# Optimization experiments

Measured on AMD Instinct MI355X. Metric: run time of the kernel, lower is better.

The kernel has to match this reference:

```python
import jax, jax.numpy as jnp
import numpy as np

# res_scale = (max(scale)+float_scale)/max(scale) = 2.5/2 = 1.25
RES_SCALE = 1.25


def _dct(x):
    # DCT-II via FFT (Makhoul), norm=None, matching torch module's dct().
    # x: [..., N]
    N = x.shape[-1]
    v = jnp.concatenate([x[..., ::2], x[..., 1::2][..., ::-1]], axis=-1)
    Vc = jnp.fft.fft(v, axis=-1)  # full FFT == _rfft(onesided=False)
    k = -jnp.arange(N, dtype=x.dtype) * (np.pi / (2.0 * N))
    V = 2.0 * (Vc.real * jnp.cos(k) - Vc.imag * jnp.sin(k))
    return V.astype(x.dtype)


def _idct(X):
    # Inverse of DCT-II (norm=None), matching torch module's idct().
    # X: [..., N]
    N = X.shape[-1]
    Xv = X / 2.0
    k = jnp.arange(N, dtype=X.dtype) * (np.pi / (2.0 * N))
    Wr, Wi = jnp.cos(k), jnp.sin(k)
    Vt_r = Xv
    Vt_i = jnp.concatenate([jnp.zeros_like(Xv[..., :1]), -Xv[..., ::-1][..., :-1]], axis=-1)
    V_r = Vt_r * Wr - Vt_i * Wi
    V_i = Vt_r * Wi + Vt_i * Wr
    # _irfft(onesided=False): keep first N//2+1 bins, irfft back to length N
    Vc = (V_r[..., : N // 2 + 1] + 1j * V_i[..., : N // 2 + 1]).astype(jnp.complex64)
    v = jnp.fft.irfft(Vc, n=N, axis=-1).astype(X.dtype)
    # odd/even de-shuffle
    x = jnp.zeros_like(v)
    x = x.at[..., ::2].set(v[..., : N - N // 2])
    x = x.at[..., 1::2].set(v[..., ::-1][..., : N // 2])
    return x


def _dct_2d(x):
    return jnp.swapaxes(_dct(jnp.swapaxes(_dct(x), -1, -2)), -1, -2)


def _idct_2d(X):
    return jnp.swapaxes(_idct(jnp.swapaxes(_idct(X), -1, -2)), -1, -2)


def setup_inputs() -> dict:
    key = jax.random.key(0)
    x = jax.random.normal(key, (16, 3, 768, 768), dtype=jnp.float32)
    return {"x": x}


def reference(x):
    B, C, H, W = x.shape
    outH, outW = int(H * RES_SCALE), int(W * RES_SCALE)
    X = _dct_2d(x)
    # ZeroPad2d((0, outW-W, 0, outH-H)): pad right and bottom with zeros
    X = jnp.pad(X, ((0, 0), (0, 0), (0, outH - H), (0, outW - W)))
    return _idct_2d(X)
```

## Files before the change

### kernel.cpp

```cpp
#include <hip/hip_runtime.h>


#define HW 768
#define OHW 960
#define NIMG 48

typedef __attribute__((ext_vector_type(8))) short short8;
typedef __attribute__((ext_vector_type(4))) float f32x4;
typedef __attribute__((ext_vector_type(4))) float float4v;
typedef __attribute__((ext_vector_type(4))) unsigned short us4;

__device__ __forceinline__ unsigned short f2bf(float f) {
    union { float f; unsigned int u; } v; v.f = f;
    unsigned int u = v.u;
    return (unsigned short)((u + 0x7FFFu + ((u >> 16) & 1u)) >> 16);
}

__device__ __forceinline__ void glds16(const void* g, void* l) {
    __builtin_amdgcn_global_load_lds(
        (const __attribute__((address_space(1))) void*)g,
        (__attribute__((address_space(3))) void*)l, 16, 0, 0);
}

__device__ __forceinline__ float dsum(int p) {
    int n1 = (767 * p) % 30720;
    int n2 = (768 * p) % 30720;
    const float w = (float)(3.14159265358979323846 / 15360.0);
    return sinf((float)n1 * w) * cosf((float)n2 * w) / sinf((float)p * w);
}

__global__ void fill_M(unsigned short* __restrict__ Mb) {
    int idx = blockIdx.x * 256 + threadIdx.x;
    if (idx >= OHW * HW) return;
    int i = idx / HW, n = idx - i * HW;
    int a = 8 * i + 4, b = 10 * n + 5;
    int p1 = a + b;
    int p2 = a - b; if (p2 < 0) p2 += 15360;
    float m = (1.0f + dsum(p1) + dsum(p2)) * (1.0f / 960.0f);
    Mb[idx] = f2bf(m);
}

__global__ void conv_bf16(const float* __restrict__ x, unsigned short* __restrict__ xb, int n4) {
    int i = blockIdx.x * 256 + threadIdx.x;
    if (i >= n4) return;
    float4v v = *(const float4v*)(x + (size_t)i * 4);
    us4 o; o.x = f2bf(v.x); o.y = f2bf(v.y); o.z = f2bf(v.z); o.w = f2bf(v.w);
    *(us4*)(xb + (size_t)i * 4) = o;
}

__global__ __launch_bounds__(256) void gemm_bt(
    const unsigned short* __restrict__ A, int lda,
    const unsigned short* __restrict__ Bg, long long strideB, int ldb,
    void* __restrict__ Cg, long long strideC, int ldc,
    int Md, int Nd, int Kd, int out_f32)
{
    __shared__ unsigned short As[128 * 32];
    __shared__ unsigned short Bs[128 * 32];

    const int tid = threadIdx.x;
    const int wave = tid >> 6, lane = tid & 63;
    const int wm = wave >> 1, wn = wave & 1;
    const int t16 = lane & 15, quad = lane >> 4;
    const int z = blockIdx.z;

    const unsigned short* B = Bg + (size_t)z * strideB;
    const int mb = blockIdx.y * 128, nbb = blockIdx.x * 128;

    f32x4 acc[4][4];
#pragma unroll
    for (int i = 0; i < 4; ++i)
#pragma unroll
        for (int j = 0; j < 4; ++j)
            acc[i][j] = (f32x4){0.f, 0.f, 0.f, 0.f};

    const int rowT = tid >> 2;
    const int ksw = (((tid & 3) ^ ((rowT >> 1) & 3)) << 3);
    unsigned short* lA0 = As + wave * 512;
    unsigned short* lB0 = Bs + wave * 512;

    int grA0 = mb + rowT;        if (grA0 >= Md) grA0 = Md - 1;
    int grA1 = mb + rowT + 64;   if (grA1 >= Md) grA1 = Md - 1;
    int gnB0 = nbb + rowT;       if (gnB0 >= Nd) gnB0 = Nd - 1;
    int gnB1 = nbb + rowT + 64;  if (gnB1 >= Nd) gnB1 = Nd - 1;
    const unsigned short* pA0 = A + (size_t)grA0 * lda + ksw;
    const unsigned short* pA1 = A + (size_t)grA1 * lda + ksw;
    const unsigned short* pB0 = B + (size_t)gnB0 * ldb + ksw;
    const unsigned short* pB1 = B + (size_t)gnB1 * ldb + ksw;

    const int quadx = quad ^ ((t16 >> 1) & 3);
    const int aBase = (wm * 64 + t16) * 32 + quadx * 8;
    const int bBase = (wn * 64 + t16) * 32 + quadx * 8;

    for (int k0 = 0; k0 < Kd; k0 += 32) {
        glds16(pA0 + k0, lA0);
        glds16(pA1 + k0, lA0 + 2048);
        glds16(pB0 + k0, lB0);
        glds16(pB1 + k0, lB0 + 2048);
        __syncthreads();

        short8 af[4], bfr[4];
#pragma unroll
        for (int mi = 0; mi < 4; ++mi)
            af[mi] = *(const short8*)(&As[aBase + mi * 512]);
#pragma unroll
        for (int ni = 0; ni < 4; ++ni)
            bfr[ni] = *(const short8*)(&Bs[bBase + ni * 512]);
#pragma unroll
        for (int mi = 0; mi < 4; ++mi)
#pragma unroll
            for (int ni = 0; ni < 4; ++ni)
                acc[mi][ni] = __builtin_amdgcn_mfma_f32_16x16x32_bf16(
                    af[mi], bfr[ni], acc[mi][ni], 0, 0, 0);
        __syncthreads();
    }

    const int gr0 = mb + wm * 64;
    const int gc0 = nbb + wn * 64;
    if (out_f32) {
        float* C = (float*)Cg + (size_t)z * strideC;
#pragma unroll
        for (int mi = 0; mi < 4; ++mi)
#pragma unroll
            for (int ni = 0; ni < 4; ++ni) {
                int col = gc0 + ni * 16 + t16;
                if (col < Nd) {
#pragma unroll
                    for (int r = 0; r < 4; ++r) {
                        int rowg = gr0 + mi * 16 + quad * 4 + r;
                        if (rowg < Md) C[(size_t)rowg * ldc + col] = acc[mi][ni][r];
                    }
                }
            }
    } else {
        unsigned short* C = (unsigned short*)Cg + (size_t)z * strideC;
#pragma unroll
        for (int mi = 0; mi < 4; ++mi)
#pragma unroll
            for (int ni = 0; ni < 4; ++ni) {
                int col = gc0 + ni * 16 + t16;
                if (col < Nd) {
#pragma unroll
                    for (int r = 0; r < 4; ++r) {
                        int rowg = gr0 + mi * 16 + quad * 4 + r;
                        if (rowg < Md) C[(size_t)rowg * ldc + col] = f2bf(acc[mi][ni][r]);
                    }
                }
            }
    }
}

extern "C" void kernel_launch(void* const* d_in, const int* in_sizes, int n_in,
                              void* d_out, int out_size, void* d_ws, size_t ws_size,
                              hipStream_t stream) {
    const float* x = (const float*)d_in[0];
    float* out = (float*)d_out;
    char* ws = (char*)d_ws;

    size_t offM  = 0;
    size_t fixed = offM + (size_t)OHW * HW * 2;
    size_t perImg = (size_t)HW * HW * 2 + (size_t)OHW * HW * 2;

    int nb = 1;
    if (ws_size > fixed + perImg) {
        size_t q = (ws_size - fixed) / perImg;
        nb = (q > 48) ? 48 : (int)q;
        if (nb < 1) nb = 1;
    }

    unsigned short* Mb = (unsigned short*)(ws + offM);
    unsigned short* xb = (unsigned short*)(ws + fixed);
    unsigned short* T  = (unsigned short*)(ws + fixed + (size_t)nb * HW * HW * 2);

    fill_M<<<(OHW * HW + 255) / 256, 256, 0, stream>>>(Mb);

    for (int b0 = 0; b0 < NIMG; b0 += nb) {
        int cur = NIMG - b0; if (cur > nb) cur = nb;
        int n4 = cur * (HW * HW / 4);
        conv_bf16<<<(n4 + 255) / 256, 256, 0, stream>>>(
            x + (size_t)b0 * HW * HW, xb, n4);
        gemm_bt<<<dim3(6, 8, cur), 256, 0, stream>>>(
            Mb, HW, xb, (long long)HW * HW, HW,
            T, (long long)OHW * HW, HW, OHW, HW, HW, 0);
        gemm_bt<<<dim3(8, 8, cur), 256, 0, stream>>>(
            Mb, HW, T, (long long)OHW * HW, HW,
            out + (size_t)b0 * OHW * OHW, (long long)OHW * OHW, OHW,
            OHW, OHW, HW, 1);
    }
    (void)in_sizes; (void)n_in; (void)out_size;
}
```

Before: 425.7 us.

## Double-buffer LDS tiles with K=64 steps in bf16 GEMM

The GEMM main loop now uses two LDS buffers with 64-wide K tiles and issues global-to-LDS loads for the next tile while MFMAs run on the current one. This halves the number of barriers per K and overlaps memory latency with compute. LDS use grows to 64 KB per block, which can lower occupancy. The loop assumes the K tile count is even, which holds for K=768.

```diff
diff --git a/kernel.cpp b/kernel.cpp
--- a/kernel.cpp
+++ b/kernel.cpp
@@ -54,8 +54,8 @@
     void* __restrict__ Cg, long long strideC, int ldc,
     int Md, int Nd, int Kd, int out_f32)
 {
-    __shared__ unsigned short As[128 * 32];
-    __shared__ unsigned short Bs[128 * 32];
+    __shared__ unsigned short As[2][128 * 64];
+    __shared__ unsigned short Bs[2][128 * 64];
 
     const int tid = threadIdx.x;
     const int wave = tid >> 6, lane = tid & 63;
@@ -63,7 +63,7 @@
     const int t16 = lane & 15, quad = lane >> 4;
     const int z = blockIdx.z;
 
-    const unsigned short* B = Bg + (size_t)z * strideB;
+    const unsigned short* Bp = Bg + (size_t)z * strideB;
     const int mb = blockIdx.y * 128, nbb = blockIdx.x * 128;
 
     f32x4 acc[4][4];
@@ -73,46 +73,74 @@
         for (int j = 0; j < 4; ++j)
             acc[i][j] = (f32x4){0.f, 0.f, 0.f, 0.f};
 
-    const int rowT = tid >> 2;
-    const int ksw = (((tid & 3) ^ ((rowT >> 1) & 3)) << 3);
-    unsigned short* lA0 = As + wave * 512;
-    unsigned short* lB0 = Bs + wave * 512;
-
-    int grA0 = mb + rowT;        if (grA0 >= Md) grA0 = Md - 1;
-    int grA1 = mb + rowT + 64;   if (grA1 >= Md) grA1 = Md - 1;
-    int gnB0 = nbb + rowT;       if (gnB0 >= Nd) gnB0 = Nd - 1;
-    int gnB1 = nbb + rowT + 64;  if (gnB1 >= Nd) gnB1 = Nd - 1;
-    const unsigned short* pA0 = A + (size_t)grA0 * lda + ksw;
-    const unsigned short* pA1 = A + (size_t)grA1 * lda + ksw;
-    const unsigned short* pB0 = B + (size_t)gnB0 * ldb + ksw;
-    const unsigned short* pB1 = B + (size_t)gnB1 * ldb + ksw;
-
-    const int quadx = quad ^ ((t16 >> 1) & 3);
-    const int aBase = (wm * 64 + t16) * 32 + quadx * 8;
-    const int bBase = (wn * 64 + t16) * 32 + quadx * 8;
-
-    for (int k0 = 0; k0 < Kd; k0 += 32) {
-        glds16(pA0 + k0, lA0);
-        glds16(pA1 + k0, lA0 + 2048);
-        glds16(pB0 + k0, lB0);
-        glds16(pB1 + k0, lB0 + 2048);
+    const int srow = tid >> 3;
+    const int klog = (((tid & 7) ^ ((tid >> 4) & 7))) * 8;
+    const unsigned short* pA[4];
+    const unsigned short* pB[4];
+#pragma unroll
+    for (int j = 0; j < 4; ++j) {
+        int ra = mb + srow + 32 * j;  if (ra >= Md) ra = Md - 1;
+        int rb = nbb + srow + 32 * j; if (rb >= Nd) rb = Nd - 1;
+        pA[j] = A  + (size_t)ra * lda + klog;
+        pB[j] = Bp + (size_t)rb * ldb + klog;
+    }
+    unsigned short* dA = &As[0][0] + tid * 8;
+    unsigned short* dB = &Bs[0][0] + tid * 8;
+
+    const int swz = (t16 >> 1) & 7;
+    int aOff[2], bOff[2];
+#pragma unroll
+    for (int ks = 0; ks < 2; ++ks) {
+        int ph = ((ks * 4 + quad) ^ swz) * 8;
+        aOff[ks] = (wm * 64 + t16) * 64 + ph;
+        bOff[ks] = (wn * 64 + t16) * 64 + ph;
+    }
+
+#define STAGE(buf, kt) do {                                                   \
+    int kk_ = (kt) * 64;                                                      \
+    _Pragma("unroll")                                                         \
+    for (int j_ = 0; j_ < 4; ++j_)                                            \
+        glds16(pA[j_] + kk_, dA + (buf) * 8192 + j_ * 2048);                  \
+    _Pragma("unroll")                                                         \
+    for (int j_ = 0; j_ < 4; ++j_)                                            \
+        glds16(pB[j_] + kk_, dB + (buf) * 8192 + j_ * 2048);                  \
+} while (0)
+
+#define COMPUTE(buf) do {                                                     \
+    _Pragma("unroll")                                                         \
+    for (int ks_ = 0; ks_ < 2; ++ks_) {                                       \
+        short8 af_[4], bf_[4];                                                \
+        _Pragma("unroll")                                                     \
+        for (int mi_ = 0; mi_ < 4; ++mi_)                                     \
+            af_[mi_] = *(const short8*)(&As[buf][0] + aOff[ks_] + mi_ * 1024);\
+        _Pragma("unroll")                                                     \
+        for (int ni_ = 0; ni_ < 4; ++ni_)                                     \
+            bf_[ni_] = *(const short8*)(&Bs[buf][0] + bOff[ks_] + ni_ * 1024);\
+        _Pragma("unroll")                                                     \
+        for (int mi_ = 0; mi_ < 4; ++mi_)                                     \
+        _Pragma("unroll")                                                     \
+        for (int ni_ = 0; ni_ < 4; ++ni_)                                     \
+            acc[mi_][ni_] = __builtin_amdgcn_mfma_f32_16x16x32_bf16(          \
+                af_[mi_], bf_[ni_], acc[mi_][ni_], 0, 0, 0);                  \
+    }                                                                         \
+} while (0)
+
+    const int NT = Kd >> 6;
+
+    STAGE(0, 0);
+    __syncthreads();
+
+    for (int kt = 0; kt + 2 <= NT; kt += 2) {
+        STAGE(1, kt + 1);
+        COMPUTE(0);
         __syncthreads();
-
-        short8 af[4], bfr[4];
-#pragma unroll
-        for (int mi = 0; mi < 4; ++mi)
-            af[mi] = *(const short8*)(&As[aBase + mi * 512]);
-#pragma unroll
-        for (int ni = 0; ni < 4; ++ni)
-            bfr[ni] = *(const short8*)(&Bs[bBase + ni * 512]);
-#pragma unroll
-        for (int mi = 0; mi < 4; ++mi)
-#pragma unroll
-            for (int ni = 0; ni < 4; ++ni)
-                acc[mi][ni] = __builtin_amdgcn_mfma_f32_16x16x32_bf16(
-                    af[mi], bfr[ni], acc[mi][ni], 0, 0, 0);
+        if (kt + 2 < NT) STAGE(0, kt + 2);
+        COMPUTE(1);
         __syncthreads();
     }
+
+#undef STAGE
+#undef COMPUTE
 
     const int gr0 = mb + wm * 64;
     const int gc0 = nbb + wn * 64;
```

Result: no change. 419.9 us (-1.4%).

## Rewrite GEMM as persistent 256x256-tile kernel with double-buffered LDS pipeline

Applied to the files above, without the earlier changes.

Replaces the 128x128 single-buffered GEMM with a persistent-grid kernel using 256x256 tiles, 512 threads, and BK=64 double-buffered LDS. Global-to-LDS loads for the next k-step, or the next tile at the end of the loop, overlap MFMA work through interleaved fragment reads, raw barriers and setprio hints. The goal is more data reuse per load and less barrier stall. In exchange it uses much more LDS and more accumulator registers. The M buffer is padded by 64 rows because the 256-row tiles read past row 960.

```diff
diff --git a/kernel.cpp b/kernel.cpp
--- a/kernel.cpp
+++ b/kernel.cpp
@@ -4,6 +4,7 @@
 #define HW 768
 #define OHW 960
 #define NIMG 48
+#define NTILES 12
 
 typedef __attribute__((ext_vector_type(8))) short short8;
 typedef __attribute__((ext_vector_type(4))) float f32x4;
@@ -48,104 +49,169 @@
     *(us4*)(xb + (size_t)i * 4) = o;
 }
 
-__global__ __launch_bounds__(256) void gemm_bt(
+#define ASM_BAR   asm volatile("s_barrier" ::: "memory")
+#define ASM_VM0   asm volatile("s_waitcnt vmcnt(0)" ::: "memory")
+
+__global__ __launch_bounds__(512, 2) void gemm_bt(
     const unsigned short* __restrict__ A, int lda,
     const unsigned short* __restrict__ Bg, long long strideB, int ldb,
     void* __restrict__ Cg, long long strideC, int ldc,
-    int Md, int Nd, int Kd, int out_f32)
+    int Md, int Nd, int out_f32, int gx, int gy, int nA)
 {
-    __shared__ unsigned short As[128 * 32];
-    __shared__ unsigned short Bs[128 * 32];
+    __shared__ unsigned short As[2][256 * 64];
+    __shared__ unsigned short Bs[2][256 * 64];
 
     const int tid = threadIdx.x;
     const int wave = tid >> 6, lane = tid & 63;
-    const int wm = wave >> 1, wn = wave & 1;
+    const int wm = wave >> 2, wn = wave & 3;
     const int t16 = lane & 15, quad = lane >> 4;
-    const int z = blockIdx.z;
-
-    const unsigned short* B = Bg + (size_t)z * strideB;
-    const int mb = blockIdx.y * 128, nbb = blockIdx.x * 128;
-
-    f32x4 acc[4][4];
-#pragma unroll
-    for (int i = 0; i < 4; ++i)
+    const int nB = gridDim.x;
+
+    int a = blockIdx.x;
+    if (a >= nA) return;
+
+    const int srow = tid >> 3;
+    const int klog = ((tid & 7) ^ ((tid >> 4) & 7)) * 8;
+    int invA[4], invB[4];
+#pragma unroll
+    for (int j = 0; j < 4; ++j) {
+        invA[j] = (srow + 64 * j) * lda + klog;
+        invB[j] = (srow + 64 * j) * ldb + klog;
+    }
+    const int dOff = tid * 8;
+
+    const int swz = (t16 >> 1) & 7;
+    const int ph0 = (quad ^ swz) * 8;
+    const int ph1 = ((4 + quad) ^ swz) * 8;
+    const int aRow = (wm * 128 + t16) * 64;
+    const int bRow = (wn * 64 + t16) * 64;
+
+    f32x4 acc[8][4];
+#pragma unroll
+    for (int i = 0; i < 8; ++i)
 #pragma unroll
         for (int j = 0; j < 4; ++j)
             acc[i][j] = (f32x4){0.f, 0.f, 0.f, 0.f};
 
-    const int rowT = tid >> 2;
-    const int ksw = (((tid & 3) ^ ((rowT >> 1) & 3)) << 3);
-    unsigned short* lA0 = As + wave * 512;
-    unsigned short* lB0 = Bs + wave * 512;
-
-    int grA0 = mb + rowT;        if (grA0 >= Md) grA0 = Md - 1;
-    int grA1 = mb + rowT + 64;   if (grA1 >= Md) grA1 = Md - 1;
-    int gnB0 = nbb + rowT;       if (gnB0 >= Nd) gnB0 = Nd - 1;
-    int gnB1 = nbb + rowT + 64;  if (gnB1 >= Nd) gnB1 = Nd - 1;
-    const unsigned short* pA0 = A + (size_t)grA0 * lda + ksw;
-    const unsigned short* pA1 = A + (size_t)grA1 * lda + ksw;
-    const unsigned short* pB0 = B + (size_t)gnB0 * ldb + ksw;
-    const unsigned short* pB1 = B + (size_t)gnB1 * ldb + ksw;
-
-    const int quadx = quad ^ ((t16 >> 1) & 3);
-    const int aBase = (wm * 64 + t16) * 32 + quadx * 8;
-    const int bBase = (wn * 64 + t16) * 32 + quadx * 8;
-
-    for (int k0 = 0; k0 < Kd; k0 += 32) {
-        glds16(pA0 + k0, lA0);
-        glds16(pA1 + k0, lA0 + 2048);
-        glds16(pB0 + k0, lB0);
-        glds16(pB1 + k0, lB0 + 2048);
-        __syncthreads();
-
-        short8 af[4], bfr[4];
-#pragma unroll
-        for (int mi = 0; mi < 4; ++mi)
-            af[mi] = *(const short8*)(&As[aBase + mi * 512]);
-#pragma unroll
-        for (int ni = 0; ni < 4; ++ni)
-            bfr[ni] = *(const short8*)(&Bs[bBase + ni * 512]);
-#pragma unroll
-        for (int mi = 0; mi < 4; ++mi)
-#pragma unroll
-            for (int ni = 0; ni < 4; ++ni)
-                acc[mi][ni] = __builtin_amdgcn_mfma_f32_16x16x32_bf16(
-                    af[mi], bfr[ni], acc[mi][ni], 0, 0, 0);
-        __syncthreads();
-    }
-
-    const int gr0 = mb + wm * 64;
-    const int gc0 = nbb + wn * 64;
-    if (out_f32) {
-        float* C = (float*)Cg + (size_t)z * strideC;
-#pragma unroll
-        for (int mi = 0; mi < 4; ++mi)
-#pragma unroll
-            for (int ni = 0; ni < 4; ++ni) {
-                int col = gc0 + ni * 16 + t16;
-                if (col < Nd) {
-#pragma unroll
-                    for (int r = 0; r < 4; ++r) {
-                        int rowg = gr0 + mi * 16 + quad * 4 + r;
-                        if (rowg < Md) C[(size_t)rowg * ldc + col] = acc[mi][ni][r];
+    int mb, nbb, zz; long long offA, offB;
+#define DECODE(aa) do { int gxy_ = gx * gy; zz = (aa) / gxy_;                  \
+    int r_ = (aa) - zz * gxy_; int by_ = r_ / gx; int bx_ = r_ - by_ * gx;     \
+    mb = by_ * 256; nbb = bx_ * 256;                                           \
+    offA = (long long)mb * lda;                                                \
+    offB = (long long)zz * strideB + (long long)nbb * ldb; } while (0)
+
+    DECODE(a);
+
+#define STG_A(buf, stk) do { _Pragma("unroll")                                 \
+    for (int j_ = 0; j_ < 4; ++j_)                                             \
+        glds16(A + offA + invA[j_] + (stk),                                    \
+               &As[buf][0] + dOff + j_ * 4096); } while (0)
+#define STG_B(buf, stk) do { _Pragma("unroll")                                 \
+    for (int j_ = 0; j_ < 4; ++j_)                                             \
+        glds16(Bg + offB + invB[j_] + (stk),                                   \
+               &Bs[buf][0] + dOff + j_ * 4096); } while (0)
+
+    short8 afr0[4][2], afr1[4][2], bf0[2][2], bf1[2][2];
+
+#define RD_A(dst, base, mig) do { _Pragma("unroll")                            \
+    for (int mi_ = 0; mi_ < 4; ++mi_) {                                        \
+        dst[mi_][0] = *(const short8*)((base) + aRow + ((mig)*4+mi_)*1024 + ph0); \
+        dst[mi_][1] = *(const short8*)((base) + aRow + ((mig)*4+mi_)*1024 + ph1); \
+    } } while (0)
+#define RD_B(dst, base, nig) do { _Pragma("unroll")                            \
+    for (int ni_ = 0; ni_ < 2; ++ni_) {                                        \
+        dst[ni_][0] = *(const short8*)((base) + bRow + ((nig)*2+ni_)*1024 + ph0); \
+        dst[ni_][1] = *(const short8*)((base) + bRow + ((nig)*2+ni_)*1024 + ph1); \
+    } } while (0)
+
+#define MMA_Q(mig, nig, av, bv) do {                                           \
+    __builtin_amdgcn_s_setprio(1);                                             \
+    _Pragma("unroll")                                                          \
+    for (int ks_ = 0; ks_ < 2; ++ks_)                                          \
+    _Pragma("unroll")                                                          \
+    for (int mi_ = 0; mi_ < 4; ++mi_)                                          \
+    _Pragma("unroll")                                                          \
+    for (int ni_ = 0; ni_ < 2; ++ni_)                                          \
+        acc[(mig)*4+mi_][(nig)*2+ni_] =                                        \
+            __builtin_amdgcn_mfma_f32_16x16x32_bf16(                           \
+                av[mi_][ks_], bv[ni_][ks_],                                    \
+                acc[(mig)*4+mi_][(nig)*2+ni_], 0, 0, 0);                       \
+    __builtin_amdgcn_s_setprio(0); } while (0)
+
+    STG_A(0, 0); STG_B(0, 0);
+    ASM_VM0; ASM_BAR;
+    RD_A(afr0, &As[0][0], 0);
+    RD_B(bf0, &Bs[0][0], 0);
+
+    for (;;) {
+        const int emb = mb, enb = nbb, ez = zz;
+#pragma unroll 2
+        for (int t = 0; t < NTILES; ++t) {
+            const int c = t & 1, n = c ^ 1;
+            const unsigned short* Asc = &As[c][0];
+            const unsigned short* Bsc = &Bs[c][0];
+            bool pf = true; int stk = (t + 1) * 64;
+            if (t == NTILES - 1) {
+                if (a + nB < nA) { DECODE(a + nB); stk = 0; }
+                else pf = false;
+            }
+            if (pf) STG_A(n, stk);
+            RD_B(bf1, Bsc, 1);
+            MMA_Q(0, 0, afr0, bf0);
+            ASM_BAR;
+            if (pf) STG_B(n, stk);
+            RD_A(afr1, Asc, 1);
+            MMA_Q(0, 1, afr0, bf1);
+            ASM_BAR;
+            MMA_Q(1, 0, afr1, bf0);
+            ASM_VM0;
+            ASM_BAR;
+            if (pf) { RD_A(afr0, &As[n][0], 0); RD_B(bf0, &Bs[n][0], 0); }
+            MMA_Q(1, 1, afr1, bf1);
+            ASM_BAR;
+        }
+
+        const int gr0 = emb + wm * 128;
+        const int gc0 = enb + wn * 64;
+        if (out_f32) {
+            float* C = (float*)Cg + (size_t)ez * strideC;
+#pragma unroll
+            for (int mi = 0; mi < 8; ++mi)
+#pragma unroll
+                for (int ni = 0; ni < 4; ++ni) {
+                    int col = gc0 + ni * 16 + t16;
+                    if (col < Nd) {
+#pragma unroll
+                        for (int r = 0; r < 4; ++r) {
+                            int rowg = gr0 + mi * 16 + quad * 4 + r;
+                            if (rowg < Md) C[(size_t)rowg * ldc + col] = acc[mi][ni][r];
+                        }
                     }
                 }
-            }
-    } else {
-        unsigned short* C = (unsigned short*)Cg + (size_t)z * strideC;
-#pragma unroll
-        for (int mi = 0; mi < 4; ++mi)
-#pragma unroll
-            for (int ni = 0; ni < 4; ++ni) {
-                int col = gc0 + ni * 16 + t16;
-                if (col < Nd) {
-#pragma unroll
-                    for (int r = 0; r < 4; ++r) {
-                        int rowg = gr0 + mi * 16 + quad * 4 + r;
-                        if (rowg < Md) C[(size_t)rowg * ldc + col] = f2bf(acc[mi][ni][r]);
+        } else {
+            unsigned short* C = (unsigned short*)Cg + (size_t)ez * strideC;
+#pragma unroll
+            for (int mi = 0; mi < 8; ++mi)
+#pragma unroll
+                for (int ni = 0; ni < 4; ++ni) {
+                    int col = gc0 + ni * 16 + t16;
+                    if (col < Nd) {
+#pragma unroll
+                        for (int r = 0; r < 4; ++r) {
+                            int rowg = gr0 + mi * 16 + quad * 4 + r;
+                            if (rowg < Md) C[(size_t)rowg * ldc + col] = f2bf(acc[mi][ni][r]);
+                        }
                     }
                 }
-            }
+        }
+
+        a += nB;
+        if (a >= nA) break;
+#pragma unroll
+        for (int i = 0; i < 8; ++i)
+#pragma unroll
+            for (int j = 0; j < 4; ++j)
+                acc[i][j] = (f32x4){0.f, 0.f, 0.f, 0.f};
     }
 }
 
@@ -156,20 +222,22 @@
     float* out = (float*)d_out;
     char* ws = (char*)d_ws;
 
-    size_t offM  = 0;
-    size_t fixed = offM + (size_t)OHW * HW * 2;
-    size_t perImg = (size_t)HW * HW * 2 + (size_t)OHW * HW * 2;
+    size_t szM   = (size_t)(OHW + 64) * HW * 2;
+    size_t fixed = szM;
+    size_t perImgX = (size_t)HW * HW * 2;
+    size_t perImgT = (size_t)OHW * HW * 2;
+    size_t padT  = (size_t)64 * HW * 2;
 
     int nb = 1;
-    if (ws_size > fixed + perImg) {
-        size_t q = (ws_size - fixed) / perImg;
+    if (ws_size > fixed + perImgX + perImgT + padT) {
+        size_t q = (ws_size - fixed - padT) / (perImgX + perImgT);
         nb = (q > 48) ? 48 : (int)q;
         if (nb < 1) nb = 1;
     }
 
-    unsigned short* Mb = (unsigned short*)(ws + offM);
+    unsigned short* Mb = (unsigned short*)(ws + 0);
     unsigned short* xb = (unsigned short*)(ws + fixed);
-    unsigned short* T  = (unsigned short*)(ws + fixed + (size_t)nb * HW * HW * 2);
+    unsigned short* T  = (unsigned short*)(ws + fixed + (size_t)nb * perImgX);
 
     fill_M<<<(OHW * HW + 255) / 256, 256, 0, stream>>>(Mb);
 
@@ -178,13 +246,21 @@
         int n4 = cur * (HW * HW / 4);
         conv_bf16<<<(n4 + 255) / 256, 256, 0, stream>>>(
             x + (size_t)b0 * HW * HW, xb, n4);
-        gemm_bt<<<dim3(6, 8, cur), 256, 0, stream>>>(
-            Mb, HW, xb, (long long)HW * HW, HW,
-            T, (long long)OHW * HW, HW, OHW, HW, HW, 0);
-        gemm_bt<<<dim3(8, 8, cur), 256, 0, stream>>>(
-            Mb, HW, T, (long long)OHW * HW, HW,
-            out + (size_t)b0 * OHW * OHW, (long long)OHW * OHW, OHW,
-            OHW, OHW, HW, 1);
+        {
+            int gx = 3, gy = 4, nA = gx * gy * cur;
+            int nblk = nA < 256 ? nA : 256;
+            gemm_bt<<<dim3(nblk), 512, 0, stream>>>(
+                Mb, HW, xb, (long long)HW * HW, HW,
+                T, (long long)OHW * HW, HW, OHW, HW, 0, gx, gy, nA);
+        }
+        {
+            int gx = 4, gy = 4, nA = gx * gy * cur;
+            int nblk = nA < 256 ? nA : 256;
+            gemm_bt<<<dim3(nblk), 512, 0, stream>>>(
+                Mb, HW, T, (long long)OHW * HW, HW,
+                out + (size_t)b0 * OHW * OHW, (long long)OHW * OHW, OHW,
+                OHW, OHW, 1, gx, gy, nA);
+        }
     }
     (void)in_sizes; (void)n_in; (void)out_size;
 }
```

Result: slower. 510.9 us (+20.0%).
